# Kernel tuning notes

Hardware: AMD Instinct MI355X
Metric: run time of the kernel (lower is better)

The kernel has to match this reference:

```python
import jax, jax.numpy as jnp
import numpy as np

DIM = 512
NUM_HEADS = 8
HEAD_DIM = DIM // NUM_HEADS
SCALE = HEAD_DIM ** -0.5


def setup_inputs() -> dict:
    key = jax.random.key(0)
    k_x, k_qkv, k_proj, k_pb = jax.random.split(key, 4)
    x = jax.random.normal(k_x, (2, 4096, DIM), dtype=jnp.float32)
    # nn.Linear weights: stored as [out, in]; qkv_bias=False so no qkv bias.
    w_qkv = jax.random.normal(k_qkv, (3 * DIM, DIM), dtype=jnp.float32) * (DIM ** -0.5)
    w_proj = jax.random.normal(k_proj, (DIM, DIM), dtype=jnp.float32) * (DIM ** -0.5)
    b_proj = jax.random.normal(k_pb, (DIM,), dtype=jnp.float32) * 0.01
    return {"x": x, "w_qkv": w_qkv, "w_proj": w_proj, "b_proj": b_proj}


def reference(x, w_qkv, w_proj, b_proj):
    B, N, D = x.shape
    H, Hd = NUM_HEADS, HEAD_DIM
    # qkv: [B, N, 3D] -> [3, B, H, N, Hd]
    qkv = (x @ w_qkv.T).reshape(B, N, 3, H, Hd).transpose(2, 0, 3, 1, 4)
    q, k, v = qkv[0], qkv[1], qkv[2]
    # Naive full attention matrix in fp32 (matches original non-fused path).
    attn = jnp.einsum('bhqd,bhkd->bhqk', q, k) * SCALE
    attn = jax.nn.softmax(attn, axis=-1)
    out = jnp.einsum('bhqk,bhkd->bhqd', attn, v)
    out = out.transpose(0, 2, 1, 3).reshape(B, N, D)
    return out @ w_proj.T + b_proj
```

## Files before the change

kernel.cpp:

```cpp
#include <hip/hip_runtime.h>
#include <stdint.h>

#define SEQ   4096
#define DIMM  512
#define HDIM  64
#define NH    8
#define ROWS  8192
#define QKVN  1536

typedef __attribute__((ext_vector_type(8))) __bf16 bf16x8;
typedef __attribute__((ext_vector_type(4))) __bf16 bf16x4;
typedef __attribute__((ext_vector_type(4))) short  shortx4;
typedef __attribute__((ext_vector_type(4))) float  f32x4;
typedef __attribute__((ext_vector_type(2))) uint32_t u32x2;

__device__ __forceinline__ uint16_t f2bfu(float f) {
  uint32_t u = __builtin_bit_cast(uint32_t, f);
  return (uint16_t)((u + 0x7FFFu + ((u >> 16) & 1u)) >> 16);
}

__device__ __forceinline__ f32x4 mfma16(bf16x8 a, bf16x8 b, f32x4 c) {
  return __builtin_amdgcn_mfma_f32_16x16x32_bf16(a, b, c, 0, 0, 0);
}

__device__ __forceinline__ f32x4 mfma16x16(bf16x4 a, bf16x4 b, f32x4 c) {
#if __has_builtin(__builtin_amdgcn_mfma_f32_16x16x16_bf16)
  return __builtin_amdgcn_mfma_f32_16x16x16_bf16(a, b, c, 0, 0, 0);
#else
  return __builtin_amdgcn_mfma_f32_16x16x16bf16_1k(
      __builtin_bit_cast(shortx4, a), __builtin_bit_cast(shortx4, b), c, 0, 0, 0);
#endif
}

#if __has_builtin(__builtin_amdgcn_exp2f)
#define EXP2F(x) __builtin_amdgcn_exp2f(x)
#else
#define EXP2F(x) exp2f(x)
#endif

__device__ __forceinline__ void gld16(const void* g, void* l) {
  __builtin_amdgcn_global_load_lds(
      (const __attribute__((address_space(1))) uint32_t*)g,
      (__attribute__((address_space(3))) uint32_t*)l, 16, 0, 0);
}

#define X4  (ROWS * DIMM / 4)
#define Q4  (QKVN * DIMM / 4)
#define P4  (DIMM * DIMM / 4)

__global__ __launch_bounds__(256) void cvt_kernel(
    const float* __restrict__ x, const float* __restrict__ wq,
    const float* __restrict__ wp, uint16_t* __restrict__ xb,
    uint16_t* __restrict__ wqb, uint16_t* __restrict__ wpb) {
  int idx = blockIdx.x * 256 + threadIdx.x;
  const float* src; uint16_t* dst; int i4;
  if (idx < X4)            { src = x;  dst = xb;  i4 = idx; }
  else if (idx < X4 + Q4)  { src = wq; dst = wqb; i4 = idx - X4; }
  else                     { src = wp; dst = wpb; i4 = idx - X4 - Q4; }
  float4 v = ((const float4*)src)[i4];
  ushort4 o;
  o.x = f2bfu(v.x); o.y = f2bfu(v.y); o.z = f2bfu(v.z); o.w = f2bfu(v.w);
  ((ushort4*)dst)[i4] = o;
}

__device__ __forceinline__ void gemm_core(
    const uint16_t* __restrict__ A, const uint16_t* __restrict__ B,
    uint16_t* As, uint16_t* Bs, f32x4 acc[4][4]) {
  const int tid = threadIdx.x;
  const int lane = tid & 63, wave = tid >> 6;
  const int quad = lane >> 4, l16 = lane & 15;
  const int wr = (wave & 1) * 64, wc = (wave >> 1) * 64;
  const int bm = blockIdx.x, bn = blockIdx.y;
  const int sw = (l16 >> 1) & 3;

  for (int kt = 0; kt < DIMM / 32; ++kt) {
#pragma unroll
    for (int it = 0; it < 2; ++it) {
      int L = it * 256 + tid;
      int r = L >> 2, c = L & 3;
      int gc = c ^ ((r >> 1) & 3);
      int ldsoff = (it * 256 + (tid & ~63)) * 16;
      gld16((const char*)A + ((size_t)(bm * 128 + r) * DIMM + kt * 32) * 2 + gc * 16,
            (char*)As + ldsoff);
      gld16((const char*)B + ((size_t)(bn * 128 + r) * DIMM + kt * 32) * 2 + gc * 16,
            (char*)Bs + ldsoff);
    }
    __syncthreads();
    bf16x8 af[4], bfr[4];
#pragma unroll
    for (int i = 0; i < 4; ++i)
      af[i] = *(const bf16x8*)(As + (wr + i * 16 + l16) * 32 + ((quad ^ sw) * 8));
#pragma unroll
    for (int j = 0; j < 4; ++j)
      bfr[j] = *(const bf16x8*)(Bs + (wc + j * 16 + l16) * 32 + ((quad ^ sw) * 8));
#pragma unroll
    for (int i = 0; i < 4; ++i)
#pragma unroll
      for (int j = 0; j < 4; ++j)
        acc[i][j] = mfma16(af[i], bfr[j], acc[i][j]);
    __syncthreads();
  }
}

__global__ __launch_bounds__(256, 2) void qk_gemm(
    const uint16_t* __restrict__ xb, const uint16_t* __restrict__ wqb,
    uint16_t* __restrict__ qd, uint16_t* __restrict__ kd) {
  __shared__ __align__(16) uint16_t As[128 * 32];
  __shared__ __align__(16) uint16_t Bs[128 * 32];
  f32x4 acc[4][4];
#pragma unroll
  for (int i = 0; i < 4; ++i)
#pragma unroll
    for (int j = 0; j < 4; ++j) acc[i][j] = f32x4{0.f, 0.f, 0.f, 0.f};

  gemm_core(wqb, xb, As, Bs, acc);

  const int lane = threadIdx.x & 63, wave = threadIdx.x >> 6;
  const int quad = lane >> 4, l16 = lane & 15;
  const int wr = (wave & 1) * 64, wc = (wave >> 1) * 64;
  const float qscale = 0.125f * 1.44269504f;
  const bool isq = (blockIdx.x < 4);
  uint16_t* dst = isq ? qd : kd;
  const float s = isq ? qscale : 1.0f;
#pragma unroll
  for (int i = 0; i < 4; ++i) {
    int jc0 = blockIdx.x * 128 + wr + i * 16 + quad * 4;
    int h = (jc0 >> 6) & 7, hd = jc0 & 63;
#pragma unroll
    for (int j = 0; j < 4; ++j) {
      int m = blockIdx.y * 128 + wc + j * 16 + l16;
      int b = m >> 12, n = m & 4095;
      int bh = (b << 3) | h;
      ushort4 pk;
      pk.x = f2bfu(acc[i][j][0] * s); pk.y = f2bfu(acc[i][j][1] * s);
      pk.z = f2bfu(acc[i][j][2] * s); pk.w = f2bfu(acc[i][j][3] * s);
      *(ushort4*)(dst + ((size_t)bh * SEQ + n) * HDIM + hd) = pk;
    }
  }
}

__global__ __launch_bounds__(256, 2) void v_gemm(
    const uint16_t* __restrict__ xb, const uint16_t* __restrict__ wvb,
    uint16_t* __restrict__ vt) {
  __shared__ __align__(16) uint16_t As[128 * 32];
  __shared__ __align__(16) uint16_t Bs[128 * 32];
  f32x4 acc[4][4];
#pragma unroll
  for (int i = 0; i < 4; ++i)
#pragma unroll
    for (int j = 0; j < 4; ++j) acc[i][j] = f32x4{0.f, 0.f, 0.f, 0.f};

  gemm_core(xb, wvb, As, Bs, acc);

  const int lane = threadIdx.x & 63, wave = threadIdx.x >> 6;
  const int quad = lane >> 4, l16 = lane & 15;
  const int wr = (wave & 1) * 64, wc = (wave >> 1) * 64;
#pragma unroll
  for (int i = 0; i < 4; ++i) {
    int m0 = blockIdx.x * 128 + wr + i * 16 + quad * 4;
    int b = m0 >> 12, n0 = m0 & 4095;
#pragma unroll
    for (int j = 0; j < 4; ++j) {
      int jcl = blockIdx.y * 128 + wc + j * 16 + l16;
      int h = (jcl >> 6) & 7, hd = jcl & 63;
      int bh = (b << 3) | h;
      ushort4 pk;
      pk.x = f2bfu(acc[i][j][0]); pk.y = f2bfu(acc[i][j][1]);
      pk.z = f2bfu(acc[i][j][2]); pk.w = f2bfu(acc[i][j][3]);
      *(ushort4*)(vt + ((size_t)bh * HDIM + hd) * SEQ + n0) = pk;
    }
  }
}

__global__ __launch_bounds__(512, 4) void attn_kernel(
    const uint16_t* __restrict__ qd, const uint16_t* __restrict__ kd,
    const uint16_t* __restrict__ vt, uint16_t* __restrict__ ao) {
  __shared__ __align__(16) uint16_t Ks[128 * 64];
  __shared__ __align__(16) uint16_t Vs[64 * 128];
  __shared__ __align__(16) f32x4 Om[4][8][64];
  __shared__ __align__(16) float2 Lb[4][64];

  const int tid = threadIdx.x, lane = tid & 63, wave = tid >> 6;
  const int quad = lane >> 4, l16 = lane & 15;
  const int pair = wave >> 1, khalf = wave & 1;
  const int qt = blockIdx.x >> 4, bh = blockIdx.x & 15;
  const size_t base_qk = (size_t)bh * SEQ * HDIM;
  const size_t base_v  = (size_t)bh * HDIM * SEQ;
  const int sw7 = l16 & 7;

  bf16x8 qf[2][2];
#pragma unroll
  for (int it2 = 0; it2 < 2; ++it2)
#pragma unroll
    for (int kh = 0; kh < 2; ++kh)
      qf[it2][kh] = *(const bf16x8*)(qd + base_qk +
          (size_t)(qt * 128 + pair * 32 + it2 * 16 + l16) * HDIM + kh * 32 + quad * 8);

  f32x4 O[2][4];
  float lsum[2] = {0.f, 0.f};
#pragma unroll
  for (int a = 0; a < 2; ++a)
#pragma unroll
    for (int d = 0; d < 4; ++d) O[a][d] = f32x4{0.f, 0.f, 0.f, 0.f};

  for (int kt = 0; kt < SEQ / 128; ++kt) {
#pragma unroll
    for (int it = 0; it < 2; ++it) {
      int L = it * 512 + tid;
      int ldsoff = (it * 512 + (tid & ~63)) * 16;
      int rk = L >> 3, ck = L & 7;
      int gck = ck ^ (rk & 7);
      gld16((const char*)kd + (base_qk + (size_t)(kt * 128 + rk) * HDIM) * 2 + gck * 16,
            (char*)Ks + ldsoff);
      int rv = L >> 4, cv = L & 15;
      int gcv = cv ^ (rv & 15);
      gld16((const char*)vt + (base_v + (size_t)rv * SEQ + (size_t)kt * 128) * 2 + gcv * 16,
            (char*)Vs + ldsoff);
    }
    __syncthreads();

    f32x4 P[4][2];
#pragma unroll
    for (int jh = 0; jh < 4; ++jh) {
      int jf = khalf * 4 + jh;
      const uint16_t* krow = Ks + (jf * 16 + l16) * 64;
      bf16x8 kf0 = *(const bf16x8*)(krow + ((quad ^ sw7) * 8));
      bf16x8 kf1 = *(const bf16x8*)(krow + (((4 + quad) ^ sw7) * 8));
#pragma unroll
      for (int it2 = 0; it2 < 2; ++it2) {
        f32x4 s = f32x4{0.f, 0.f, 0.f, 0.f};
        s = mfma16(kf0, qf[it2][0], s);
        s = mfma16(kf1, qf[it2][1], s);
        P[jh][it2] = s;
      }
    }

#pragma unroll
    for (int jh = 0; jh < 4; ++jh) {
      bf16x4 pb[2];
#pragma unroll
      for (int it2 = 0; it2 < 2; ++it2) {
        float p0 = EXP2F(P[jh][it2][0]);
        float p1 = EXP2F(P[jh][it2][1]);
        float p2 = EXP2F(P[jh][it2][2]);
        float p3 = EXP2F(P[jh][it2][3]);
        lsum[it2] += (p0 + p1) + (p2 + p3);
        uint32_t a0 = __builtin_bit_cast(uint32_t, p0) + 0x8000u;
        uint32_t a1 = __builtin_bit_cast(uint32_t, p1) + 0x8000u;
        uint32_t a2 = __builtin_bit_cast(uint32_t, p2) + 0x8000u;
        uint32_t a3 = __builtin_bit_cast(uint32_t, p3) + 0x8000u;
        u32x2 pk;
        pk.x = (a0 >> 16) | (a1 & 0xFFFF0000u);
        pk.y = (a2 >> 16) | (a3 & 0xFFFF0000u);
        pb[it2] = __builtin_bit_cast(bf16x4, pk);
      }
      int c = khalf * 8 + jh * 2 + (quad >> 1);
      int coff = ((c ^ l16) * 16) + (quad & 1) * 8;
#pragma unroll
      for (int dl = 0; dl < 4; ++dl) {
        bf16x4 va = *(const bf16x4*)((const char*)Vs + (dl * 16 + l16) * 256 + coff);
#pragma unroll
        for (int it2 = 0; it2 < 2; ++it2)
          O[it2][dl] = mfma16x16(va, pb[it2], O[it2][dl]);
      }
    }
    __syncthreads();
  }

  if (!(wave & 1)) {
#pragma unroll
    for (int it2 = 0; it2 < 2; ++it2)
#pragma unroll
      for (int dl = 0; dl < 4; ++dl)
        Om[pair][it2 * 4 + dl][lane] = O[it2][dl];
    Lb[pair][lane] = make_float2(lsum[0], lsum[1]);
  }
  __syncthreads();
  if (wave & 1) {
    float2 lp = Lb[pair][lane];
    lsum[0] += lp.x; lsum[1] += lp.y;
#pragma unroll
    for (int it2 = 0; it2 < 2; ++it2)
#pragma unroll
      for (int dl = 0; dl < 4; ++dl)
        O[it2][dl] += Om[pair][it2 * 4 + dl][lane];

    const int b = bh >> 3, h = bh & 7;
#pragma unroll
    for (int it2 = 0; it2 < 2; ++it2) {
      float l = lsum[it2];
      l += __shfl_xor(l, 16);
      l += __shfl_xor(l, 32);
      float inv = 1.0f / l;
      int q = qt * 128 + pair * 32 + it2 * 16 + l16;
      size_t rowbase = ((size_t)(b * SEQ + q)) * DIMM + h * HDIM;
#pragma unroll
      for (int dl = 0; dl < 4; ++dl) {
        ushort4 pk;
        pk.x = f2bfu(O[it2][dl][0] * inv);
        pk.y = f2bfu(O[it2][dl][1] * inv);
        pk.z = f2bfu(O[it2][dl][2] * inv);
        pk.w = f2bfu(O[it2][dl][3] * inv);
        *(ushort4*)(ao + rowbase + dl * 16 + quad * 4) = pk;
      }
    }
  }
}

__global__ __launch_bounds__(256, 2) void proj_gemm(
    const uint16_t* __restrict__ ao, const uint16_t* __restrict__ wpb,
    const float* __restrict__ bprj, float* __restrict__ out) {
  __shared__ __align__(16) uint16_t As[128 * 32];
  __shared__ __align__(16) uint16_t Bs[128 * 32];
  f32x4 acc[4][4];
#pragma unroll
  for (int i = 0; i < 4; ++i)
#pragma unroll
    for (int j = 0; j < 4; ++j) acc[i][j] = f32x4{0.f, 0.f, 0.f, 0.f};

  gemm_core(wpb, ao, As, Bs, acc);

  const int lane = threadIdx.x & 63, wave = threadIdx.x >> 6;
  const int quad = lane >> 4, l16 = lane & 15;
  const int wr = (wave & 1) * 64, wc = (wave >> 1) * 64;
#pragma unroll
  for (int i = 0; i < 4; ++i) {
    int jc0 = blockIdx.x * 128 + wr + i * 16 + quad * 4;
    float4 b4 = *(const float4*)(bprj + jc0);
#pragma unroll
    for (int j = 0; j < 4; ++j) {
      int m = blockIdx.y * 128 + wc + j * 16 + l16;
      float4 o;
      o.x = acc[i][j][0] + b4.x; o.y = acc[i][j][1] + b4.y;
      o.z = acc[i][j][2] + b4.z; o.w = acc[i][j][3] + b4.w;
      *(float4*)(out + (size_t)m * DIMM + jc0) = o;
    }
  }
}

extern "C" void kernel_launch(void* const* d_in, const int* in_sizes, int n_in,
                              void* d_out, int out_size, void* d_ws, size_t ws_size,
                              hipStream_t stream) {
  const float* x     = (const float*)d_in[0];
  const float* wqkv  = (const float*)d_in[1];
  const float* wproj = (const float*)d_in[2];
  const float* bproj = (const float*)d_in[3];

  char* ws = (char*)d_ws;
  uint16_t* xb  = (uint16_t*)(ws + 0);
  uint16_t* wqb = (uint16_t*)(ws + 8388608);
  uint16_t* wpb = (uint16_t*)(ws + 9961472);
  uint16_t* qd  = (uint16_t*)(ws + 10485760);
  uint16_t* kd  = (uint16_t*)(ws + 18874368);
  uint16_t* vt  = (uint16_t*)(ws + 27262976);
  uint16_t* ao  = (uint16_t*)(ws + 35651584);

  cvt_kernel<<<(X4 + Q4 + P4) / 256, 256, 0, stream>>>(x, wqkv, wproj, xb, wqb, wpb);
  qk_gemm<<<dim3(8, 64), 256, 0, stream>>>(xb, wqb, qd, kd);
  v_gemm<<<dim3(64, 4), 256, 0, stream>>>(xb, wqb + 1024 * DIMM, vt);
  attn_kernel<<<512, 512, 0, stream>>>(qd, kd, vt, ao);
  proj_gemm<<<dim3(4, 64), 256, 0, stream>>>(ao, wpb, bproj, (float*)d_out);
}
```

Measured before the change: 205.0 us.

## Merge QK and V GEMMs into one launch; double attention key tile to 256

Combines the QK and V projection GEMMs into a single 768-block launch with a 1-D block index decoded per branch, raising the occupancy hint to 3. This removes one launch and the tail between the two kernels. The attention kernel now processes 256 keys per iteration instead of 128, which halves the barriers and loop trips, and it fuses the exp/pack step directly after each score MFMA. The merge buffer reuses the K tile's shared memory to fit the larger tiles. The larger LDS footprint may lower attention occupancy.

```diff
diff --git a/kernel.cpp b/kernel.cpp
--- a/kernel.cpp
+++ b/kernel.cpp
@@ -65,12 +65,11 @@
 
 __device__ __forceinline__ void gemm_core(
     const uint16_t* __restrict__ A, const uint16_t* __restrict__ B,
-    uint16_t* As, uint16_t* Bs, f32x4 acc[4][4]) {
+    uint16_t* As, uint16_t* Bs, f32x4 acc[4][4], int bm, int bn) {
   const int tid = threadIdx.x;
   const int lane = tid & 63, wave = tid >> 6;
   const int quad = lane >> 4, l16 = lane & 15;
   const int wr = (wave & 1) * 64, wc = (wave >> 1) * 64;
-  const int bm = blockIdx.x, bn = blockIdx.y;
   const int sw = (l16 >> 1) & 3;
 
   for (int kt = 0; kt < DIMM / 32; ++kt) {
@@ -102,45 +101,9 @@
   }
 }
 
-__global__ __launch_bounds__(256, 2) void qk_gemm(
+__global__ __launch_bounds__(256, 3) void qkv_gemm2(
     const uint16_t* __restrict__ xb, const uint16_t* __restrict__ wqb,
-    uint16_t* __restrict__ qd, uint16_t* __restrict__ kd) {
-  __shared__ __align__(16) uint16_t As[128 * 32];
-  __shared__ __align__(16) uint16_t Bs[128 * 32];
-  f32x4 acc[4][4];
-#pragma unroll
-  for (int i = 0; i < 4; ++i)
-#pragma unroll
-    for (int j = 0; j < 4; ++j) acc[i][j] = f32x4{0.f, 0.f, 0.f, 0.f};
-
-  gemm_core(wqb, xb, As, Bs, acc);
-
-  const int lane = threadIdx.x & 63, wave = threadIdx.x >> 6;
-  const int quad = lane >> 4, l16 = lane & 15;
-  const int wr = (wave & 1) * 64, wc = (wave >> 1) * 64;
-  const float qscale = 0.125f * 1.44269504f;
-  const bool isq = (blockIdx.x < 4);
-  uint16_t* dst = isq ? qd : kd;
-  const float s = isq ? qscale : 1.0f;
-#pragma unroll
-  for (int i = 0; i < 4; ++i) {
-    int jc0 = blockIdx.x * 128 + wr + i * 16 + quad * 4;
-    int h = (jc0 >> 6) & 7, hd = jc0 & 63;
-#pragma unroll
-    for (int j = 0; j < 4; ++j) {
-      int m = blockIdx.y * 128 + wc + j * 16 + l16;
-      int b = m >> 12, n = m & 4095;
-      int bh = (b << 3) | h;
-      ushort4 pk;
-      pk.x = f2bfu(acc[i][j][0] * s); pk.y = f2bfu(acc[i][j][1] * s);
-      pk.z = f2bfu(acc[i][j][2] * s); pk.w = f2bfu(acc[i][j][3] * s);
-      *(ushort4*)(dst + ((size_t)bh * SEQ + n) * HDIM + hd) = pk;
-    }
-  }
-}
-
-__global__ __launch_bounds__(256, 2) void v_gemm(
-    const uint16_t* __restrict__ xb, const uint16_t* __restrict__ wvb,
+    uint16_t* __restrict__ qd, uint16_t* __restrict__ kd,
     uint16_t* __restrict__ vt) {
   __shared__ __align__(16) uint16_t As[128 * 32];
   __shared__ __align__(16) uint16_t Bs[128 * 32];
@@ -150,24 +113,51 @@
 #pragma unroll
     for (int j = 0; j < 4; ++j) acc[i][j] = f32x4{0.f, 0.f, 0.f, 0.f};
 
-  gemm_core(xb, wvb, As, Bs, acc);
-
   const int lane = threadIdx.x & 63, wave = threadIdx.x >> 6;
   const int quad = lane >> 4, l16 = lane & 15;
   const int wr = (wave & 1) * 64, wc = (wave >> 1) * 64;
-#pragma unroll
-  for (int i = 0; i < 4; ++i) {
-    int m0 = blockIdx.x * 128 + wr + i * 16 + quad * 4;
-    int b = m0 >> 12, n0 = m0 & 4095;
-#pragma unroll
-    for (int j = 0; j < 4; ++j) {
-      int jcl = blockIdx.y * 128 + wc + j * 16 + l16;
-      int h = (jcl >> 6) & 7, hd = jcl & 63;
-      int bh = (b << 3) | h;
-      ushort4 pk;
-      pk.x = f2bfu(acc[i][j][0]); pk.y = f2bfu(acc[i][j][1]);
-      pk.z = f2bfu(acc[i][j][2]); pk.w = f2bfu(acc[i][j][3]);
-      *(ushort4*)(vt + ((size_t)bh * HDIM + hd) * SEQ + n0) = pk;
+  const int blk = blockIdx.x;
+
+  if (blk < 512) {
+    int bm = blk & 7, bn = blk >> 3;
+    gemm_core(wqb, xb, As, Bs, acc, bm, bn);
+    const float qscale = 0.125f * 1.44269504f;
+    const bool isq = (bm < 4);
+    uint16_t* dst = isq ? qd : kd;
+    const float s = isq ? qscale : 1.0f;
+#pragma unroll
+    for (int i = 0; i < 4; ++i) {
+      int jc0 = bm * 128 + wr + i * 16 + quad * 4;
+      int h = (jc0 >> 6) & 7, hd = jc0 & 63;
+#pragma unroll
+      for (int j = 0; j < 4; ++j) {
+        int m = bn * 128 + wc + j * 16 + l16;
+        int b = m >> 12, n = m & 4095;
+        int bh = (b << 3) | h;
+        ushort4 pk;
+        pk.x = f2bfu(acc[i][j][0] * s); pk.y = f2bfu(acc[i][j][1] * s);
+        pk.z = f2bfu(acc[i][j][2] * s); pk.w = f2bfu(acc[i][j][3] * s);
+        *(ushort4*)(dst + ((size_t)bh * SEQ + n) * HDIM + hd) = pk;
+      }
+    }
+  } else {
+    int idx = blk - 512;
+    int bm = idx >> 2, bn = idx & 3;
+    gemm_core(xb, wqb + 1024 * DIMM, As, Bs, acc, bm, bn);
+#pragma unroll
+    for (int i = 0; i < 4; ++i) {
+      int m0 = bm * 128 + wr + i * 16 + quad * 4;
+      int b = m0 >> 12, n0 = m0 & 4095;
+#pragma unroll
+      for (int j = 0; j < 4; ++j) {
+        int jcl = bn * 128 + wc + j * 16 + l16;
+        int h = (jcl >> 6) & 7, hd = jcl & 63;
+        int bh = (b << 3) | h;
+        ushort4 pk;
+        pk.x = f2bfu(acc[i][j][0]); pk.y = f2bfu(acc[i][j][1]);
+        pk.z = f2bfu(acc[i][j][2]); pk.w = f2bfu(acc[i][j][3]);
+        *(ushort4*)(vt + ((size_t)bh * HDIM + hd) * SEQ + n0) = pk;
+      }
     }
   }
 }
@@ -175,9 +165,8 @@
 __global__ __launch_bounds__(512, 4) void attn_kernel(
     const uint16_t* __restrict__ qd, const uint16_t* __restrict__ kd,
     const uint16_t* __restrict__ vt, uint16_t* __restrict__ ao) {
-  __shared__ __align__(16) uint16_t Ks[128 * 64];
-  __shared__ __align__(16) uint16_t Vs[64 * 128];
-  __shared__ __align__(16) f32x4 Om[4][8][64];
+  __shared__ __align__(16) uint16_t Ks[256 * 64];
+  __shared__ __align__(16) uint16_t Vs[64 * 256];
   __shared__ __align__(16) float2 Lb[4][64];
 
   const int tid = threadIdx.x, lane = tid & 63, wave = tid >> 6;
@@ -203,47 +192,38 @@
 #pragma unroll
     for (int d = 0; d < 4; ++d) O[a][d] = f32x4{0.f, 0.f, 0.f, 0.f};
 
-  for (int kt = 0; kt < SEQ / 128; ++kt) {
-#pragma unroll
-    for (int it = 0; it < 2; ++it) {
+  for (int kt = 0; kt < SEQ / 256; ++kt) {
+#pragma unroll
+    for (int it = 0; it < 4; ++it) {
       int L = it * 512 + tid;
       int ldsoff = (it * 512 + (tid & ~63)) * 16;
       int rk = L >> 3, ck = L & 7;
       int gck = ck ^ (rk & 7);
-      gld16((const char*)kd + (base_qk + (size_t)(kt * 128 + rk) * HDIM) * 2 + gck * 16,
+      gld16((const char*)kd + (base_qk + (size_t)(kt * 256 + rk) * HDIM) * 2 + gck * 16,
             (char*)Ks + ldsoff);
-      int rv = L >> 4, cv = L & 15;
-      int gcv = cv ^ (rv & 15);
-      gld16((const char*)vt + (base_v + (size_t)rv * SEQ + (size_t)kt * 128) * 2 + gcv * 16,
+      int rv = L >> 5, cv = L & 31;
+      int gcv = cv ^ (rv & 31);
+      gld16((const char*)vt + (base_v + (size_t)rv * SEQ + (size_t)kt * 256) * 2 + gcv * 16,
             (char*)Vs + ldsoff);
     }
     __syncthreads();
 
-    f32x4 P[4][2];
-#pragma unroll
-    for (int jh = 0; jh < 4; ++jh) {
-      int jf = khalf * 4 + jh;
+#pragma unroll
+    for (int jh = 0; jh < 8; ++jh) {
+      int jf = khalf * 8 + jh;
       const uint16_t* krow = Ks + (jf * 16 + l16) * 64;
       bf16x8 kf0 = *(const bf16x8*)(krow + ((quad ^ sw7) * 8));
       bf16x8 kf1 = *(const bf16x8*)(krow + (((4 + quad) ^ sw7) * 8));
+      bf16x4 pb[2];
 #pragma unroll
       for (int it2 = 0; it2 < 2; ++it2) {
         f32x4 s = f32x4{0.f, 0.f, 0.f, 0.f};
         s = mfma16(kf0, qf[it2][0], s);
         s = mfma16(kf1, qf[it2][1], s);
-        P[jh][it2] = s;
-      }
-    }
-
-#pragma unroll
-    for (int jh = 0; jh < 4; ++jh) {
-      bf16x4 pb[2];
-#pragma unroll
-      for (int it2 = 0; it2 < 2; ++it2) {
-        float p0 = EXP2F(P[jh][it2][0]);
-        float p1 = EXP2F(P[jh][it2][1]);
-        float p2 = EXP2F(P[jh][it2][2]);
-        float p3 = EXP2F(P[jh][it2][3]);
+        float p0 = EXP2F(s[0]);
+        float p1 = EXP2F(s[1]);
+        float p2 = EXP2F(s[2]);
+        float p3 = EXP2F(s[3]);
         lsum[it2] += (p0 + p1) + (p2 + p3);
         uint32_t a0 = __builtin_bit_cast(uint32_t, p0) + 0x8000u;
         uint32_t a1 = __builtin_bit_cast(uint32_t, p1) + 0x8000u;
@@ -254,11 +234,12 @@
         pk.y = (a2 >> 16) | (a3 & 0xFFFF0000u);
         pb[it2] = __builtin_bit_cast(bf16x4, pk);
       }
-      int c = khalf * 8 + jh * 2 + (quad >> 1);
-      int coff = ((c ^ l16) * 16) + (quad & 1) * 8;
+      int c = khalf * 16 + jh * 2 + (quad >> 1);
 #pragma unroll
       for (int dl = 0; dl < 4; ++dl) {
-        bf16x4 va = *(const bf16x4*)((const char*)Vs + (dl * 16 + l16) * 256 + coff);
+        int rowkey = ((dl & 1) << 4) | l16;
+        bf16x4 va = *(const bf16x4*)((const char*)Vs + (dl * 16 + l16) * 512 +
+                                     ((c ^ rowkey) * 16) + (quad & 1) * 8);
 #pragma unroll
         for (int it2 = 0; it2 < 2; ++it2)
           O[it2][dl] = mfma16x16(va, pb[it2], O[it2][dl]);
@@ -267,12 +248,13 @@
     __syncthreads();
   }
 
+  f32x4* Om = (f32x4*)Ks;
   if (!(wave & 1)) {
 #pragma unroll
     for (int it2 = 0; it2 < 2; ++it2)
 #pragma unroll
       for (int dl = 0; dl < 4; ++dl)
-        Om[pair][it2 * 4 + dl][lane] = O[it2][dl];
+        Om[(pair * 8 + it2 * 4 + dl) * 64 + lane] = O[it2][dl];
     Lb[pair][lane] = make_float2(lsum[0], lsum[1]);
   }
   __syncthreads();
@@ -283,7 +265,7 @@
     for (int it2 = 0; it2 < 2; ++it2)
 #pragma unroll
       for (int dl = 0; dl < 4; ++dl)
-        O[it2][dl] += Om[pair][it2 * 4 + dl][lane];
+        O[it2][dl] += Om[(pair * 8 + it2 * 4 + dl) * 64 + lane];
 
     const int b = bh >> 3, h = bh & 7;
 #pragma unroll
@@ -318,7 +300,7 @@
 #pragma unroll
     for (int j = 0; j < 4; ++j) acc[i][j] = f32x4{0.f, 0.f, 0.f, 0.f};
 
-  gemm_core(wpb, ao, As, Bs, acc);
+  gemm_core(wpb, ao, As, Bs, acc, blockIdx.x, blockIdx.y);
 
   const int lane = threadIdx.x & 63, wave = threadIdx.x >> 6;
   const int quad = lane >> 4, l16 = lane & 15;
@@ -356,8 +338,7 @@
   uint16_t* ao  = (uint16_t*)(ws + 35651584);
 
   cvt_kernel<<<(X4 + Q4 + P4) / 256, 256, 0, stream>>>(x, wqkv, wproj, xb, wqb, wpb);
-  qk_gemm<<<dim3(8, 64), 256, 0, stream>>>(xb, wqb, qd, kd);
-  v_gemm<<<dim3(64, 4), 256, 0, stream>>>(xb, wqb + 1024 * DIMM, vt);
+  qkv_gemm2<<<768, 256, 0, stream>>>(xb, wqb, qd, kd, vt);
   attn_kernel<<<512, 512, 0, stream>>>(qd, kd, vt, ao);
   proj_gemm<<<dim3(4, 64), 256, 0, stream>>>(ao, wpb, bproj, (float*)d_out);
 }
```

New measurement: 297.1 us. +44.9%, slower.
